# Kernel tuning notes

Measured on AMD Instinct MI355X. Metric: run time of the kernel, lower is better.

## Reference

```python
import jax, jax.numpy as jnp
import numpy as np

N0, N1, N2, N3 = 50000, 25000, 25000, 25000
D = 128
E = 800000
E12 = 400000


def scatter_mean(src, idx, n):
    # torch_scatter.scatter_mean: sum / clamp(count, min=1)
    s = jax.ops.segment_sum(src, idx, num_segments=n)
    c = jax.ops.segment_sum(jnp.ones((src.shape[0],), src.dtype), idx, num_segments=n)
    return s / jnp.maximum(c, 1.0)[:, None]


def setup_inputs() -> dict:
    key = jax.random.key(0)
    ks = jax.random.split(key, 32)
    sc = 1.0 / np.sqrt(D)
    inp = {}
    inp['x_node'] = jax.random.normal(ks[0], (N0, D), jnp.float32)
    inp['x1'] = jax.random.normal(ks[1], (N1, D), jnp.float32)
    inp['x2'] = jax.random.normal(ks[2], (N2, D), jnp.float32)
    inp['x3'] = jax.random.normal(ks[3], (N3, D), jnp.float32)
    inp['w1'] = jax.random.uniform(ks[4], (E,), jnp.float32)
    inp['w2'] = jax.random.uniform(ks[5], (E,), jnp.float32)
    inp['w3'] = jax.random.uniform(ks[6], (E,), jnp.float32)
    inp['W1'] = jax.random.normal(ks[7], (D, D), jnp.float32) * sc
    inp['b1'] = jnp.zeros((D,), jnp.float32)
    inp['W2'] = jax.random.normal(ks[8], (D, D), jnp.float32) * sc
    inp['b2'] = jnp.zeros((D,), jnp.float32)
    inp['W3'] = jax.random.normal(ks[9], (D, D), jnp.float32) * sc
    inp['b3'] = jnp.zeros((D,), jnp.float32)
    inp['W121'] = jax.random.normal(ks[10], (D, D), jnp.float32) * sc
    inp['b121'] = jnp.zeros((D,), jnp.float32)
    inp['W131'] = jax.random.normal(ks[11], (D, D), jnp.float32) * sc
    inp['b131'] = jnp.zeros((D,), jnp.float32)
    inp['att_vec'] = jax.random.normal(ks[12], (5, D), jnp.float32) * sc
    inp['e1_src'] = jax.random.randint(ks[13], (E,), 0, N0, jnp.int32)
    inp['e1_dst'] = jax.random.randint(ks[14], (E,), 0, N1, jnp.int32)
    inp['e2_src'] = jax.random.randint(ks[15], (E,), 0, N0, jnp.int32)
    inp['e2_dst'] = jax.random.randint(ks[16], (E,), 0, N2, jnp.int32)
    inp['e3_src'] = jax.random.randint(ks[17], (E,), 0, N0, jnp.int32)
    inp['e3_dst'] = jax.random.randint(ks[18], (E,), 0, N3, jnp.int32)
    inp['e12_src'] = jax.random.randint(ks[19], (E12,), 0, N1, jnp.int32)
    inp['e12_dst'] = jax.random.randint(ks[20], (E12,), 0, N2, jnp.int32)
    inp['e13_src'] = jax.random.randint(ks[21], (E12,), 0, N1, jnp.int32)
    inp['e13_dst'] = jax.random.randint(ks[22], (E12,), 0, N3, jnp.int32)
    return inp


def reference(x_node, x1, x2, x3, w1, w2, w3, W1, b1, W2, b2, W3, b3,
              W121, b121, W131, b131, att_vec,
              e1_src, e1_dst, e2_src, e2_dst, e3_src, e3_dst,
              e12_src, e12_dst, e13_src, e13_dst):
    n0 = x_node.shape[0]

    def lin_relu(x, W, b):
        return jax.nn.relu(x @ W.T + b)

    def short_path(xm, w, src, dst):
        # s -> t (weighted scatter_mean), combine, t -> s (scatter_mean)
        msg = scatter_mean(x_node[src] * w[:, None], dst, xm.shape[0])
        net = (msg + xm) * 0.5
        return scatter_mean(net[dst], src, n0)

    s1s = lin_relu(short_path(x1, w1, e1_src, e1_dst), W1, b1)
    s2s = lin_relu(short_path(x2, w2, e2_src, e2_dst), W2, b2)
    s3s = lin_relu(short_path(x3, w3, e3_src, e3_dst), W3, b3)

    # shared first hop for s-1-2-1-s and s-1-3-1-s (identical in the source)
    net1 = (scatter_mean(x_node[e1_src] * w1[:, None], e1_dst, x1.shape[0]) + x1) * 0.5

    def long_path(xm, em_src, em_dst):
        m2 = scatter_mean(net1[em_src], em_dst, xm.shape[0])
        n2 = (m2 + xm) * 0.5
        m3 = scatter_mean(n2[em_dst], em_src, x1.shape[0])
        n3 = (m3 + x1) * 0.5
        return scatter_mean(n3[e1_dst] * w1[:, None], e1_src, n0)

    s121s = lin_relu(long_path(x2, e12_src, e12_dst), W121, b121)
    s131s = lin_relu(long_path(x3, e13_src, e13_dst), W131, b131)

    allm = jnp.stack([s1s, s2s, s3s, s121s, s131s], axis=1)  # [N0, 5, D]
    scores = jnp.einsum('npd,pd->np', allm, att_vec)         # [N0, 5]
    att = jax.nn.softmax(scores, axis=1)
    return jnp.einsum('npd,np->nd', allm, att)               # [N0, D]
```

## Files before the change

kernel.cpp:

```cpp
#include <hip/hip_runtime.h>
#include <cmath>

static constexpr int FD = 128;
static constexpr int NCSR = 10;

struct HistArgs {
    const int* key[NCSR];
    int* deg[NCSR];
    int E[NCSR];
    int blkOff[NCSR + 1];
};
__global__ __launch_bounds__(256) void k_hist_all(HistArgs a) {
    int b = blockIdx.x;
    int c = 0;
    while (b >= a.blkOff[c + 1]) ++c;
    int e = (b - a.blkOff[c]) * 256 + threadIdx.x;
    if (e < a.E[c]) atomicAdd(&a.deg[c][a.key[c][e]], 1);
}

struct ScanArgs {
    const int* deg[NCSR];
    int* rowptr[NCSR];
    int* cursor[NCSR];
    int N[NCSR];
};
__global__ __launch_bounds__(1024) void k_scan(ScanArgs a) {
    const int which = blockIdx.x;
    const int* deg = a.deg[which];
    int* rowptr = a.rowptr[which];
    int* cursor = a.cursor[which];
    const int N = a.N[which];
    __shared__ int wsum[16];
    __shared__ int carry_s;
    int t = threadIdx.x, lane = t & 63, wid = t >> 6;
    if (t == 0) { carry_s = 0; rowptr[0] = 0; }
    __syncthreads();
    for (int base = 0; base < N; base += 1024) {
        int i = base + t;
        int v = (i < N) ? deg[i] : 0;
        int s = v;
#pragma unroll
        for (int off = 1; off < 64; off <<= 1) {
            int u = __shfl_up(s, off);
            if (lane >= off) s += u;
        }
        __syncthreads();
        if (lane == 63) wsum[wid] = s;
        __syncthreads();
        if (wid == 0) {
            int ws = (lane < 16) ? wsum[lane] : 0;
#pragma unroll
            for (int off = 1; off < 16; off <<= 1) {
                int u = __shfl_up(ws, off);
                if (lane >= off) ws += u;
            }
            if (lane < 16) wsum[lane] = ws;
        }
        __syncthreads();
        int waveoff = wid ? wsum[wid - 1] : 0;
        int total = wsum[15];
        int mycarry = carry_s;
        int incl = mycarry + waveoff + s;
        if (i < N) {
            rowptr[i + 1] = incl;
            cursor[i] = incl - v;
        }
        __syncthreads();
        if (t == 0) carry_s = mycarry + total;
    }
}

struct FillArgs {
    const int* key[NCSR];
    const int* val[NCSR];
    const float* w[NCSR];
    int* cursor[NCSR];
    int* dst[NCSR];
    int E[NCSR];
    int blkOff[NCSR + 1];
    int paired[NCSR];
};
__global__ __launch_bounds__(256) void k_fill_all(FillArgs a) {
    int b = blockIdx.x;
    int c = 0;
    while (b >= a.blkOff[c + 1]) ++c;
    int e = (b - a.blkOff[c]) * 256 + threadIdx.x;
    if (e >= a.E[c]) return;
    int pos = atomicAdd(&a.cursor[c][a.key[c][e]], 1);
    if (a.paired[c]) {
        int2 p;
        p.x = a.val[c][e];
        p.y = __float_as_int(a.w[c][e]);
        reinterpret_cast<int2*>(a.dst[c])[pos] = p;
    } else {
        a.dst[c][pos] = a.val[c][e];
    }
}

__global__ __launch_bounds__(256) void k_gather_w(const float* __restrict__ feat,
                                                  const int2* __restrict__ pairs,
                                                  const int* __restrict__ rowptr,
                                                  const float* __restrict__ xm,
                                                  float* __restrict__ out, int N) {
    int n = blockIdx.x * 4 + (threadIdx.x >> 6);
    if (n >= N) return;
    int lane = threadIdx.x & 63;
    int start = rowptr[n], end = rowptr[n + 1];
    float2 acc = make_float2(0.f, 0.f);
    for (int base = start; base < end; base += 64) {
        int cnt = min(64, end - base);
        int2 mp = (base + lane < end) ? pairs[base + lane] : make_int2(0, 0);
        int k = 0;
        for (; k + 4 <= cnt; k += 4) {
            int s0 = __shfl(mp.x, k),     s1 = __shfl(mp.x, k + 1);
            int s2 = __shfl(mp.x, k + 2), s3 = __shfl(mp.x, k + 3);
            float w0 = __int_as_float(__shfl(mp.y, k));
            float w1 = __int_as_float(__shfl(mp.y, k + 1));
            float w2 = __int_as_float(__shfl(mp.y, k + 2));
            float w3 = __int_as_float(__shfl(mp.y, k + 3));
            float2 v0 = *reinterpret_cast<const float2*>(&feat[(size_t)s0 * FD + lane * 2]);
            float2 v1 = *reinterpret_cast<const float2*>(&feat[(size_t)s1 * FD + lane * 2]);
            float2 v2 = *reinterpret_cast<const float2*>(&feat[(size_t)s2 * FD + lane * 2]);
            float2 v3 = *reinterpret_cast<const float2*>(&feat[(size_t)s3 * FD + lane * 2]);
            acc.x += v0.x * w0 + v1.x * w1 + v2.x * w2 + v3.x * w3;
            acc.y += v0.y * w0 + v1.y * w1 + v2.y * w2 + v3.y * w3;
        }
        for (; k < cnt; ++k) {
            int s = __shfl(mp.x, k);
            float w = __int_as_float(__shfl(mp.y, k));
            float2 v = *reinterpret_cast<const float2*>(&feat[(size_t)s * FD + lane * 2]);
            acc.x += v.x * w;
            acc.y += v.y * w;
        }
    }
    float inv = 1.0f / fmaxf((float)(end - start), 1.0f);
    size_t o = (size_t)n * FD + lane * 2;
    float2 r;
    if (xm) {
        const float2 x = *reinterpret_cast<const float2*>(&xm[o]);
        r.x = (acc.x * inv + x.x) * 0.5f;
        r.y = (acc.y * inv + x.y) * 0.5f;
    } else {
        r.x = acc.x * inv;
        r.y = acc.y * inv;
    }
    *reinterpret_cast<float2*>(&out[o]) = r;
}

__global__ __launch_bounds__(256) void k_gather_u(const float* __restrict__ feat,
                                                  const int* __restrict__ csr_src,
                                                  const int* __restrict__ rowptr,
                                                  const float* __restrict__ xm,
                                                  float* __restrict__ out, int N) {
    int n = blockIdx.x * 4 + (threadIdx.x >> 6);
    if (n >= N) return;
    int lane = threadIdx.x & 63;
    int start = rowptr[n], end = rowptr[n + 1];
    float2 acc = make_float2(0.f, 0.f);
    for (int base = start; base < end; base += 64) {
        int cnt = min(64, end - base);
        int myi = (base + lane < end) ? csr_src[base + lane] : 0;
        int k = 0;
        for (; k + 4 <= cnt; k += 4) {
            int s0 = __shfl(myi, k),     s1 = __shfl(myi, k + 1);
            int s2 = __shfl(myi, k + 2), s3 = __shfl(myi, k + 3);
            float2 v0 = *reinterpret_cast<const float2*>(&feat[(size_t)s0 * FD + lane * 2]);
            float2 v1 = *reinterpret_cast<const float2*>(&feat[(size_t)s1 * FD + lane * 2]);
            float2 v2 = *reinterpret_cast<const float2*>(&feat[(size_t)s2 * FD + lane * 2]);
            float2 v3 = *reinterpret_cast<const float2*>(&feat[(size_t)s3 * FD + lane * 2]);
            acc.x += v0.x + v1.x + v2.x + v3.x;
            acc.y += v0.y + v1.y + v2.y + v3.y;
        }
        for (; k < cnt; ++k) {
            int s = __shfl(myi, k);
            float2 v = *reinterpret_cast<const float2*>(&feat[(size_t)s * FD + lane * 2]);
            acc.x += v.x;
            acc.y += v.y;
        }
    }
    float inv = 1.0f / fmaxf((float)(end - start), 1.0f);
    size_t o = (size_t)n * FD + lane * 2;
    float2 r;
    if (xm) {
        const float2 x = *reinterpret_cast<const float2*>(&xm[o]);
        r.x = (acc.x * inv + x.x) * 0.5f;
        r.y = (acc.y * inv + x.y) * 0.5f;
    } else {
        r.x = acc.x * inv;
        r.y = acc.y * inv;
    }
    *reinterpret_cast<float2*>(&out[o]) = r;
}

__global__ __launch_bounds__(256) void k_gather3_w(const float* __restrict__ f1,
                                                   const float* __restrict__ f2,
                                                   const float* __restrict__ f3,
                                                   const int2* __restrict__ pairs,
                                                   const int* __restrict__ rowptr,
                                                   float* __restrict__ o1,
                                                   float* __restrict__ o2,
                                                   float* __restrict__ o3, int N) {
    int n = blockIdx.x * 4 + (threadIdx.x >> 6);
    if (n >= N) return;
    int lane = threadIdx.x & 63;
    int start = rowptr[n], end = rowptr[n + 1];
    float2 a1 = make_float2(0.f, 0.f), a2 = a1, a3 = a1;
    for (int base = start; base < end; base += 64) {
        int cnt = min(64, end - base);
        int2 mp = (base + lane < end) ? pairs[base + lane] : make_int2(0, 0);
        int k = 0;
        for (; k + 2 <= cnt; k += 2) {
            int sA = __shfl(mp.x, k), sB = __shfl(mp.x, k + 1);
            float wA = __int_as_float(__shfl(mp.y, k));
            float wB = __int_as_float(__shfl(mp.y, k + 1));
            size_t oA = (size_t)sA * FD + lane * 2;
            size_t oB = (size_t)sB * FD + lane * 2;
            float2 v1A = *reinterpret_cast<const float2*>(&f1[oA]);
            float2 v2A = *reinterpret_cast<const float2*>(&f2[oA]);
            float2 v3A = *reinterpret_cast<const float2*>(&f3[oA]);
            float2 v1B = *reinterpret_cast<const float2*>(&f1[oB]);
            float2 v2B = *reinterpret_cast<const float2*>(&f2[oB]);
            float2 v3B = *reinterpret_cast<const float2*>(&f3[oB]);
            a1.x += v1A.x + v1B.x;            a1.y += v1A.y + v1B.y;
            a2.x += v2A.x * wA + v2B.x * wB;  a2.y += v2A.y * wA + v2B.y * wB;
            a3.x += v3A.x * wA + v3B.x * wB;  a3.y += v3A.y * wA + v3B.y * wB;
        }
        for (; k < cnt; ++k) {
            int s = __shfl(mp.x, k);
            float w = __int_as_float(__shfl(mp.y, k));
            size_t oo = (size_t)s * FD + lane * 2;
            float2 v1 = *reinterpret_cast<const float2*>(&f1[oo]);
            float2 v2 = *reinterpret_cast<const float2*>(&f2[oo]);
            float2 v3 = *reinterpret_cast<const float2*>(&f3[oo]);
            a1.x += v1.x;      a1.y += v1.y;
            a2.x += v2.x * w;  a2.y += v2.y * w;
            a3.x += v3.x * w;  a3.y += v3.y * w;
        }
    }
    float inv = 1.0f / fmaxf((float)(end - start), 1.0f);
    size_t o = (size_t)n * FD + lane * 2;
    *reinterpret_cast<float2*>(&o1[o]) = make_float2(a1.x * inv, a1.y * inv);
    *reinterpret_cast<float2*>(&o2[o]) = make_float2(a2.x * inv, a2.y * inv);
    *reinterpret_cast<float2*>(&o3[o]) = make_float2(a3.x * inv, a3.y * inv);
}

__global__ __launch_bounds__(256) void k_linrelu2(float* __restrict__ xio,
                                                  const float* __restrict__ W,
                                                  const float* __restrict__ b, int N) {
    __shared__ float Wl[128 * 128];
    __shared__ float xs[32][128];
    const int t = threadIdx.x;
#pragma unroll
    for (int q = 0; q < 16; ++q) {
        int lin = (q * 256 + t) * 4;
        int o = lin >> 7;
        int i = lin & 127;
        float4 wv = *reinterpret_cast<const float4*>(&W[lin]);
        int sw = o & 15;
        int k0 = (i >> 1) ^ sw;
        int k1 = ((i >> 1) + 1) ^ sw;
        *reinterpret_cast<float2*>(&Wl[o * 128 + (k0 << 1)]) = make_float2(wv.x, wv.y);
        *reinterpret_cast<float2*>(&Wl[o * 128 + (k1 << 1)]) = make_float2(wv.z, wv.w);
    }
    const int oc = t & 31;
    const int rg = t >> 5;
    const int sw = oc & 15;
    float bias[4] = {b[oc], b[oc + 32], b[oc + 64], b[oc + 96]};

    const int ntiles = (N + 31) >> 5;
    for (int tile = blockIdx.x; tile < ntiles; tile += gridDim.x) {
        const int row0 = tile << 5;
        __syncthreads();
        {
            int r = t >> 3;
            int c = (t & 7) * 16;
            int row = row0 + r;
            float4* dst = reinterpret_cast<float4*>(&xs[r][c]);
            if (row < N) {
                const float4* src = reinterpret_cast<const float4*>(&xio[(size_t)row * FD + c]);
                dst[0] = src[0]; dst[1] = src[1]; dst[2] = src[2]; dst[3] = src[3];
            } else {
                float4 z = make_float4(0.f, 0.f, 0.f, 0.f);
                dst[0] = z; dst[1] = z; dst[2] = z; dst[3] = z;
            }
        }
        __syncthreads();
        float acc[4][4];
#pragma unroll
        for (int j = 0; j < 4; ++j)
#pragma unroll
            for (int c = 0; c < 4; ++c) acc[j][c] = bias[c];
#pragma unroll 8
        for (int c2 = 0; c2 < 64; ++c2) {
            int wcol = ((c2 ^ sw) << 1);
            float2 w0 = *reinterpret_cast<const float2*>(&Wl[(oc     ) * 128 + wcol]);
            float2 w1 = *reinterpret_cast<const float2*>(&Wl[(oc + 32) * 128 + wcol]);
            float2 w2 = *reinterpret_cast<const float2*>(&Wl[(oc + 64) * 128 + wcol]);
            float2 w3 = *reinterpret_cast<const float2*>(&Wl[(oc + 96) * 128 + wcol]);
            int xcol = c2 << 1;
            float2 x0 = *reinterpret_cast<const float2*>(&xs[rg * 4 + 0][xcol]);
            float2 x1 = *reinterpret_cast<const float2*>(&xs[rg * 4 + 1][xcol]);
            float2 x2 = *reinterpret_cast<const float2*>(&xs[rg * 4 + 2][xcol]);
            float2 x3 = *reinterpret_cast<const float2*>(&xs[rg * 4 + 3][xcol]);
            acc[0][0] += x0.x * w0.x + x0.y * w0.y;
            acc[0][1] += x0.x * w1.x + x0.y * w1.y;
            acc[0][2] += x0.x * w2.x + x0.y * w2.y;
            acc[0][3] += x0.x * w3.x + x0.y * w3.y;
            acc[1][0] += x1.x * w0.x + x1.y * w0.y;
            acc[1][1] += x1.x * w1.x + x1.y * w1.y;
            acc[1][2] += x1.x * w2.x + x1.y * w2.y;
            acc[1][3] += x1.x * w3.x + x1.y * w3.y;
            acc[2][0] += x2.x * w0.x + x2.y * w0.y;
            acc[2][1] += x2.x * w1.x + x2.y * w1.y;
            acc[2][2] += x2.x * w2.x + x2.y * w2.y;
            acc[2][3] += x2.x * w3.x + x2.y * w3.y;
            acc[3][0] += x3.x * w0.x + x3.y * w0.y;
            acc[3][1] += x3.x * w1.x + x3.y * w1.y;
            acc[3][2] += x3.x * w2.x + x3.y * w2.y;
            acc[3][3] += x3.x * w3.x + x3.y * w3.y;
        }
#pragma unroll
        for (int j = 0; j < 4; ++j) {
            int row = row0 + rg * 4 + j;
            if (row < N) {
                size_t base = (size_t)row * FD;
                xio[base + oc]      = fmaxf(acc[j][0], 0.f);
                xio[base + oc + 32] = fmaxf(acc[j][1], 0.f);
                xio[base + oc + 64] = fmaxf(acc[j][2], 0.f);
                xio[base + oc + 96] = fmaxf(acc[j][3], 0.f);
            }
        }
    }
}

__global__ __launch_bounds__(128) void k_att(const float* __restrict__ s0, const float* __restrict__ s1,
                                             const float* __restrict__ s2, const float* __restrict__ s3,
                                             const float* __restrict__ s4, const float* __restrict__ attv,
                                             float* __restrict__ out, int N0) {
    int n = blockIdx.x;
    int d = threadIdx.x;
    size_t base = (size_t)n * FD + d;
    float a0 = s0[base], a1 = s1[base], a2 = s2[base], a3 = s3[base], a4 = s4[base];
    float part[5];
    part[0] = a0 * attv[0 * FD + d];
    part[1] = a1 * attv[1 * FD + d];
    part[2] = a2 * attv[2 * FD + d];
    part[3] = a3 * attv[3 * FD + d];
    part[4] = a4 * attv[4 * FD + d];
    __shared__ float red[5][2];
    int lane = d & 63, wv = d >> 6;
#pragma unroll
    for (int p = 0; p < 5; ++p) {
        float v = part[p];
#pragma unroll
        for (int off = 32; off >= 1; off >>= 1) v += __shfl_down(v, off);
        if (lane == 0) red[p][wv] = v;
    }
    __syncthreads();
    float sc[5], m = -1e30f, ssum = 0.f;
#pragma unroll
    for (int p = 0; p < 5; ++p) { sc[p] = red[p][0] + red[p][1]; m = fmaxf(m, sc[p]); }
#pragma unroll
    for (int p = 0; p < 5; ++p) { sc[p] = __expf(sc[p] - m); ssum += sc[p]; }
    float inv = 1.0f / ssum;
    out[base] = (a0 * sc[0] + a1 * sc[1] + a2 * sc[2] + a3 * sc[3] + a4 * sc[4]) * inv;
}

extern "C" void kernel_launch(void* const* d_in, const int* in_sizes, int n_in,
                              void* d_out, int out_size, void* d_ws, size_t ws_size,
                              hipStream_t stream) {
    const float* x_node = (const float*)d_in[0];
    const float* x1 = (const float*)d_in[1];
    const float* x2 = (const float*)d_in[2];
    const float* x3 = (const float*)d_in[3];
    const float* w1 = (const float*)d_in[4];
    const float* w2 = (const float*)d_in[5];
    const float* w3 = (const float*)d_in[6];
    const float* W1 = (const float*)d_in[7];
    const float* b1 = (const float*)d_in[8];
    const float* W2 = (const float*)d_in[9];
    const float* b2 = (const float*)d_in[10];
    const float* W3 = (const float*)d_in[11];
    const float* b3 = (const float*)d_in[12];
    const float* W121 = (const float*)d_in[13];
    const float* b121 = (const float*)d_in[14];
    const float* W131 = (const float*)d_in[15];
    const float* b131 = (const float*)d_in[16];
    const float* attv = (const float*)d_in[17];
    const int* e1s = (const int*)d_in[18];
    const int* e1d = (const int*)d_in[19];
    const int* e2s = (const int*)d_in[20];
    const int* e2d = (const int*)d_in[21];
    const int* e3s = (const int*)d_in[22];
    const int* e3d = (const int*)d_in[23];
    const int* e12s = (const int*)d_in[24];
    const int* e12d = (const int*)d_in[25];
    const int* e13s = (const int*)d_in[26];
    const int* e13d = (const int*)d_in[27];

    const int N0 = in_sizes[0] / FD;
    const int N1 = in_sizes[1] / FD;
    const int N2 = in_sizes[2] / FD;
    const int N3 = in_sizes[3] / FD;
    const int E = in_sizes[4];
    const int E12 = in_sizes[24];

    char* wsb = (char*)d_ws;
    size_t off = 0;
    auto alloc_f = [&](size_t n) { float* p = (float*)(wsb + off); off += n * 4; return p; };
    auto alloc_i = [&](size_t n) { int* p = (int*)(wsb + off); off += n * 4; return p; };

    float* s1s  = alloc_f((size_t)N0 * FD);
    float* s2s  = alloc_f((size_t)N0 * FD);
    float* s3s  = alloc_f((size_t)N0 * FD);
    float* s121 = alloc_f((size_t)N0 * FD);
    float* s131 = alloc_f((size_t)N0 * FD);
    float* net1 = alloc_f((size_t)N1 * FD);
    float* A2   = alloc_f((size_t)N2 * FD);
    float* A3   = alloc_f((size_t)N3 * FD);
    float* B12  = alloc_f((size_t)N1 * FD);
    float* B13  = alloc_f((size_t)N1 * FD);

    const int   csrN[NCSR]    = {N1, N2, N3, N0, N0, N0, N2, N1, N3, N1};
    const int   csrE[NCSR]    = {E, E, E, E, E, E, E12, E12, E12, E12};
    const int*  csrKey[NCSR]  = {e1d, e2d, e3d, e1s, e2s, e3s, e12d, e12s, e13d, e13s};
    const int*  csrVal[NCSR]  = {e1s, e2s, e3s, e1d, e2d, e3d, e12s, e12d, e13s, e13d};
    const float* csrWin[NCSR] = {w1, w2, w3, w1, nullptr, nullptr, nullptr, nullptr, nullptr, nullptr};

    size_t degStart = off;
    int* deg[NCSR]; int* rowptr[NCSR]; int* cursor[NCSR]; int* dst[NCSR];
    for (int c = 0; c < NCSR; ++c) deg[c] = alloc_i(csrN[c]);
    size_t degBytes = off - degStart;
    for (int c = 0; c < NCSR; ++c) rowptr[c] = alloc_i(csrN[c] + 1);
    for (int c = 0; c < NCSR; ++c) cursor[c] = alloc_i(csrN[c]);
    for (int c = 0; c < NCSR; ++c) dst[c] = alloc_i(csrWin[c] ? (size_t)csrE[c] * 2 : (size_t)csrE[c]);

    const int TB = 256;
    auto cdiv = [](long long a, long long b) { return (int)((a + b - 1) / b); };

    hipMemsetAsync((void*)deg[0], 0, degBytes, stream);

    HistArgs ha;
    FillArgs fa;
    int boff = 0;
    for (int c = 0; c < NCSR; ++c) {
        ha.key[c] = csrKey[c]; ha.deg[c] = deg[c]; ha.E[c] = csrE[c];
        fa.key[c] = csrKey[c]; fa.val[c] = csrVal[c]; fa.w[c] = csrWin[c];
        fa.cursor[c] = cursor[c]; fa.dst[c] = dst[c]; fa.E[c] = csrE[c];
        fa.paired[c] = csrWin[c] ? 1 : 0;
        ha.blkOff[c] = boff; fa.blkOff[c] = boff;
        boff += cdiv(csrE[c], TB);
    }
    ha.blkOff[NCSR] = boff; fa.blkOff[NCSR] = boff;

    k_hist_all<<<boff, TB, 0, stream>>>(ha);
    ScanArgs sa;
    for (int c = 0; c < NCSR; ++c) { sa.deg[c] = deg[c]; sa.rowptr[c] = rowptr[c]; sa.cursor[c] = cursor[c]; sa.N[c] = csrN[c]; }
    k_scan<<<NCSR, 1024, 0, stream>>>(sa);
    k_fill_all<<<boff, TB, 0, stream>>>(fa);

    auto gw = [&](const float* feat, int c, const float* xm, float* out, int N) {
        k_gather_w<<<cdiv(N, 4), 256, 0, stream>>>(feat, (const int2*)dst[c], rowptr[c], xm, out, N);
    };
    auto gu = [&](const float* feat, int c, const float* xm, float* out, int N) {
        k_gather_u<<<cdiv(N, 4), 256, 0, stream>>>(feat, dst[c], rowptr[c], xm, out, N);
    };
    auto linrelu = [&](float* xio, const float* W, const float* b) {
        int ntiles = (N0 + 31) >> 5;
        int grid = ntiles < 512 ? ntiles : 512;
        k_linrelu2<<<grid, 256, 0, stream>>>(xio, W, b, N0);
    };

    gw(x_node, 0, x1, net1, N1);
    gw(x_node, 1, x2, A2, N2);
    gw(x_node, 2, x3, A3, N3);

    gu(A2, 4, nullptr, s2s, N0);
    gu(A3, 5, nullptr, s3s, N0);

    gu(net1, 6, x2, A2, N2);
    gu(A2, 7, x1, B12, N1);
    gu(net1, 8, x3, A3, N3);
    gu(A3, 9, x1, B13, N1);

    k_gather3_w<<<cdiv(N0, 4), 256, 0, stream>>>(net1, B12, B13, (const int2*)dst[3],
                                                 rowptr[3], s1s, s121, s131, N0);

    linrelu(s1s, W1, b1);
    linrelu(s2s, W2, b2);
    linrelu(s3s, W3, b3);
    linrelu(s121, W121, b121);
    linrelu(s131, W131, b131);

    k_att<<<N0, FD, 0, stream>>>(s1s, s2s, s3s, s121, s131, attv, (float*)d_out, N0);
}
```

Baseline: 1.709 ms.

## Replace atomic CSR fill with two-pass bucketed binning through a staging buffer

The single CSR fill kernel, which did scattered atomic cursor increments and writes over the whole edge array, is replaced by two passes. Pass A groups edges into 256-row buckets, using shared-memory histograms and per-bucket global cursors computed in the scan, and writes key/val/weight records to a staging area. Pass B processes one bucket per block so that the cursor atomics and destination writes stay localized. This trades extra staging traffic (16 bytes per edge, written and then read back) and one more launch for better locality in the fill. The staging area reuses the feature-buffer region of the workspace before those buffers are written.

```diff
diff --git a/kernel.cpp b/kernel.cpp
--- a/kernel.cpp
+++ b/kernel.cpp
@@ -3,6 +3,7 @@
 
 static constexpr int FD = 128;
 static constexpr int NCSR = 10;
+static constexpr int TILE_A = 2048;
 
 struct HistArgs {
     const int* key[NCSR];
@@ -22,6 +23,7 @@
     const int* deg[NCSR];
     int* rowptr[NCSR];
     int* cursor[NCSR];
+    int* bcur[NCSR];
     int N[NCSR];
 };
 __global__ __launch_bounds__(1024) void k_scan(ScanArgs a) {
@@ -29,6 +31,7 @@
     const int* deg = a.deg[which];
     int* rowptr = a.rowptr[which];
     int* cursor = a.cursor[which];
+    int* bcur = a.bcur[which];
     const int N = a.N[which];
     __shared__ int wsum[16];
     __shared__ int carry_s;
@@ -62,38 +65,94 @@
         int mycarry = carry_s;
         int incl = mycarry + waveoff + s;
         if (i < N) {
+            int rstart = incl - v;
             rowptr[i + 1] = incl;
-            cursor[i] = incl - v;
+            cursor[i] = rstart;
+            if ((i & 255) == 0) bcur[i >> 8] = rstart;
         }
         __syncthreads();
         if (t == 0) carry_s = mycarry + total;
     }
 }
 
-struct FillArgs {
+struct BinAArgs {
     const int* key[NCSR];
     const int* val[NCSR];
     const float* w[NCSR];
-    int* cursor[NCSR];
-    int* dst[NCSR];
+    int* bcur[NCSR];
+    int4* stage[NCSR];
     int E[NCSR];
     int blkOff[NCSR + 1];
     int paired[NCSR];
 };
-__global__ __launch_bounds__(256) void k_fill_all(FillArgs a) {
+__global__ __launch_bounds__(256) void k_binA(BinAArgs a) {
+    __shared__ int hist[256];
+    __shared__ int lcnt[256];
+    __shared__ int gbase[256];
     int b = blockIdx.x;
     int c = 0;
     while (b >= a.blkOff[c + 1]) ++c;
-    int e = (b - a.blkOff[c]) * 256 + threadIdx.x;
-    if (e >= a.E[c]) return;
-    int pos = atomicAdd(&a.cursor[c][a.key[c][e]], 1);
-    if (a.paired[c]) {
-        int2 p;
-        p.x = a.val[c][e];
-        p.y = __float_as_int(a.w[c][e]);
-        reinterpret_cast<int2*>(a.dst[c])[pos] = p;
-    } else {
-        a.dst[c][pos] = a.val[c][e];
+    int e0 = (b - a.blkOff[c]) * TILE_A;
+    int t = threadIdx.x;
+    int E = a.E[c];
+    hist[t] = 0; lcnt[t] = 0;
+    __syncthreads();
+    int key[8];
+#pragma unroll
+    for (int k = 0; k < 8; ++k) {
+        int e = e0 + k * 256 + t;
+        key[k] = (e < E) ? a.key[c][e] : -1;
+        if (key[k] >= 0) atomicAdd(&hist[key[k] >> 8], 1);
+    }
+    __syncthreads();
+    if (hist[t] > 0) gbase[t] = atomicAdd(&a.bcur[c][t], hist[t]);
+    __syncthreads();
+    const int* val = a.val[c];
+    const float* w = a.w[c];
+    int4* stage = a.stage[c];
+    int paired = a.paired[c];
+#pragma unroll
+    for (int k = 0; k < 8; ++k) {
+        if (key[k] < 0) continue;
+        int e = e0 + k * 256 + t;
+        int bk = key[k] >> 8;
+        int loff = atomicAdd(&lcnt[bk], 1);
+        int4 rec;
+        rec.x = key[k];
+        rec.y = val[e];
+        rec.z = paired ? __float_as_int(w[e]) : 0;
+        rec.w = 0;
+        stage[gbase[bk] + loff] = rec;
+    }
+}
+
+struct BinBArgs {
+    const int4* stage[NCSR];
+    const int* rowptr[NCSR];
+    int* cursor[NCSR];
+    int* dst[NCSR];
+    int N[NCSR];
+    int blkOff[NCSR + 1];
+    int paired[NCSR];
+};
+__global__ __launch_bounds__(256) void k_binB(BinBArgs a) {
+    int b = blockIdx.x;
+    int c = 0;
+    while (b >= a.blkOff[c + 1]) ++c;
+    int bk = b - a.blkOff[c];
+    int r0 = bk << 8;
+    int r1 = min(r0 + 256, a.N[c]);
+    int sbeg = a.rowptr[c][r0];
+    int send = a.rowptr[c][r1];
+    const int4* stage = a.stage[c];
+    int* cursor = a.cursor[c];
+    int* dst = a.dst[c];
+    int paired = a.paired[c];
+    for (int s = sbeg + (int)threadIdx.x; s < send; s += 256) {
+        int4 rec = stage[s];
+        int pos = atomicAdd(&cursor[rec.x], 1);
+        if (paired) reinterpret_cast<int2*>(dst)[pos] = make_int2(rec.y, rec.z);
+        else dst[pos] = rec.y;
     }
 }
 
@@ -420,6 +479,7 @@
     float* A3   = alloc_f((size_t)N3 * FD);
     float* B12  = alloc_f((size_t)N1 * FD);
     float* B13  = alloc_f((size_t)N1 * FD);
+    size_t featureBytes = off;
 
     const int   csrN[NCSR]    = {N1, N2, N3, N0, N0, N0, N2, N1, N3, N1};
     const int   csrE[NCSR]    = {E, E, E, E, E, E, E12, E12, E12, E12};
@@ -428,12 +488,20 @@
     const float* csrWin[NCSR] = {w1, w2, w3, w1, nullptr, nullptr, nullptr, nullptr, nullptr, nullptr};
 
     size_t degStart = off;
-    int* deg[NCSR]; int* rowptr[NCSR]; int* cursor[NCSR]; int* dst[NCSR];
+    int* deg[NCSR]; int* rowptr[NCSR]; int* cursor[NCSR]; int* bcur[NCSR]; int* dst[NCSR];
     for (int c = 0; c < NCSR; ++c) deg[c] = alloc_i(csrN[c]);
     size_t degBytes = off - degStart;
     for (int c = 0; c < NCSR; ++c) rowptr[c] = alloc_i(csrN[c] + 1);
     for (int c = 0; c < NCSR; ++c) cursor[c] = alloc_i(csrN[c]);
+    for (int c = 0; c < NCSR; ++c) bcur[c] = alloc_i(((csrN[c] + 255) >> 8));
     for (int c = 0; c < NCSR; ++c) dst[c] = alloc_i(csrWin[c] ? (size_t)csrE[c] * 2 : (size_t)csrE[c]);
+
+    int4* stage[NCSR];
+    {
+        size_t soff = 0;
+        for (int c = 0; c < NCSR; ++c) { stage[c] = (int4*)(wsb + soff); soff += (size_t)csrE[c] * 16; }
+        (void)featureBytes;
+    }
 
     const int TB = 256;
     auto cdiv = [](long long a, long long b) { return (int)((a + b - 1) / b); };
@@ -441,23 +509,45 @@
     hipMemsetAsync((void*)deg[0], 0, degBytes, stream);
 
     HistArgs ha;
-    FillArgs fa;
     int boff = 0;
     for (int c = 0; c < NCSR; ++c) {
         ha.key[c] = csrKey[c]; ha.deg[c] = deg[c]; ha.E[c] = csrE[c];
-        fa.key[c] = csrKey[c]; fa.val[c] = csrVal[c]; fa.w[c] = csrWin[c];
-        fa.cursor[c] = cursor[c]; fa.dst[c] = dst[c]; fa.E[c] = csrE[c];
-        fa.paired[c] = csrWin[c] ? 1 : 0;
-        ha.blkOff[c] = boff; fa.blkOff[c] = boff;
+        ha.blkOff[c] = boff;
         boff += cdiv(csrE[c], TB);
     }
-    ha.blkOff[NCSR] = boff; fa.blkOff[NCSR] = boff;
-
+    ha.blkOff[NCSR] = boff;
     k_hist_all<<<boff, TB, 0, stream>>>(ha);
+
     ScanArgs sa;
-    for (int c = 0; c < NCSR; ++c) { sa.deg[c] = deg[c]; sa.rowptr[c] = rowptr[c]; sa.cursor[c] = cursor[c]; sa.N[c] = csrN[c]; }
+    for (int c = 0; c < NCSR; ++c) {
+        sa.deg[c] = deg[c]; sa.rowptr[c] = rowptr[c]; sa.cursor[c] = cursor[c];
+        sa.bcur[c] = bcur[c]; sa.N[c] = csrN[c];
+    }
     k_scan<<<NCSR, 1024, 0, stream>>>(sa);
-    k_fill_all<<<boff, TB, 0, stream>>>(fa);
+
+    BinAArgs baa;
+    int aoff = 0;
+    for (int c = 0; c < NCSR; ++c) {
+        baa.key[c] = csrKey[c]; baa.val[c] = csrVal[c]; baa.w[c] = csrWin[c];
+        baa.bcur[c] = bcur[c]; baa.stage[c] = stage[c]; baa.E[c] = csrE[c];
+        baa.paired[c] = csrWin[c] ? 1 : 0;
+        baa.blkOff[c] = aoff;
+        aoff += cdiv(csrE[c], TILE_A);
+    }
+    baa.blkOff[NCSR] = aoff;
+    k_binA<<<aoff, TB, 0, stream>>>(baa);
+
+    BinBArgs bab;
+    int bboff = 0;
+    for (int c = 0; c < NCSR; ++c) {
+        bab.stage[c] = stage[c]; bab.rowptr[c] = rowptr[c]; bab.cursor[c] = cursor[c];
+        bab.dst[c] = dst[c]; bab.N[c] = csrN[c];
+        bab.paired[c] = csrWin[c] ? 1 : 0;
+        bab.blkOff[c] = bboff;
+        bboff += (csrN[c] + 255) >> 8;
+    }
+    bab.blkOff[NCSR] = bboff;
+    k_binB<<<bboff, TB, 0, stream>>>(bab);
 
     auto gw = [&](const float* feat, int c, const float* xm, float* out, int N) {
         k_gather_w<<<cdiv(N, 4), 256, 0, stream>>>(feat, (const int2*)dst[c], rowptr[c], xm, out, N);
```

Result: faster. 1.446 ms (-15.4%).
